# Kernel tuning notes

Hardware: AMD Instinct MI355X
Metric: run time of the kernel (lower is better)

Reference implementation:

```python
import jax, jax.numpy as jnp
import numpy as np

B, T, C = 4, 2048, 2048
H, KV, HD = 16, 4, 128  # n_head, n_kv_head, head_dim
G = H // KV             # query heads per kv head


def _rope(t, cos, sin):
    # t: [B, T, h, HD]; cos/sin: [T, HD//2] -> broadcast as [1, T, 1, HD//2]
    tr = t.reshape(t.shape[:-1] + (HD // 2, 2))
    t_r, t_i = tr[..., 0], tr[..., 1]
    c = cos[None, :, None, :]
    s = sin[None, :, None, :]
    o_r = t_r * c - t_i * s
    o_i = t_r * s + t_i * c
    return jnp.stack((o_r, o_i), axis=-1).reshape(t.shape)


def setup_inputs() -> dict:
    key = jax.random.key(0)
    ks = jax.random.split(key, 7)
    sc = 0.02
    return {
        "x": jax.random.normal(ks[0], (B, T, C), jnp.float32),
        "cos_freqs": jnp.cos(jnp.outer(jnp.arange(T, dtype=jnp.float32),
                                       1.0 / (10000.0 ** (jnp.arange(HD // 2, dtype=jnp.float32) * 2 / HD)))),
        "sin_freqs": jnp.sin(jnp.outer(jnp.arange(T, dtype=jnp.float32),
                                       1.0 / (10000.0 ** (jnp.arange(HD // 2, dtype=jnp.float32) * 2 / HD)))),
        "wq": jax.random.normal(ks[1], (H * HD, C), jnp.float32) * sc,
        "wk": jax.random.normal(ks[2], (KV * HD, C), jnp.float32) * sc,
        "wv": jax.random.normal(ks[3], (KV * HD, C), jnp.float32) * sc,
        "wo": jax.random.normal(ks[4], (C, H * HD), jnp.float32) * sc,
    }


def reference(x, cos_freqs, sin_freqs, wq, wk, wv, wo):
    # projections (Linear with bias=False: y = x @ W.T)
    q = (x @ wq.T).reshape(B, T, H, HD)
    k = (x @ wk.T).reshape(B, T, KV, HD)
    v = (x @ wv.T).reshape(B, T, KV, HD)
    q, k = _rope(q, cos_freqs, sin_freqs), _rope(k, cos_freqs, sin_freqs)
    # GQA attention without materializing repeated K/V: group q heads per kv head
    qg = q.reshape(B, T, KV, G, HD).transpose(0, 2, 3, 1, 4)  # [B,KV,G,T,HD]
    kh = k.transpose(0, 2, 1, 3)                              # [B,KV,T,HD]
    vh = v.transpose(0, 2, 1, 3)                              # [B,KV,T,HD]
    scale = 1.0 / jnp.sqrt(jnp.float32(HD))
    scores = jnp.einsum('bkgtd,bksd->bkgts', qg, kh) * scale  # [B,KV,G,T,T]
    mask = jnp.tril(jnp.ones((T, T), dtype=bool))
    scores = jnp.where(mask, scores, jnp.float32(-jnp.inf))
    attn = jax.nn.softmax(scores, axis=-1)
    out = jnp.einsum('bkgts,bksd->bkgtd', attn, vh)           # [B,KV,G,T,HD]
    out = out.transpose(0, 3, 1, 2, 4).reshape(B, T, H * HD)
    return out @ wo.T
```

## Files before the change

kernel.cpp:

```cpp
#include <hip/hip_runtime.h>
#include <hip/hip_bf16.h>
#include <math.h>

typedef __attribute__((ext_vector_type(8))) short short8;
typedef __attribute__((ext_vector_type(4))) float floatx4;

__device__ __forceinline__ float bf2f(unsigned short u) {
  union { unsigned int i; float f; } x; x.i = ((unsigned int)u) << 16; return x.f;
}
__device__ __forceinline__ unsigned short f2bf(float f) {
  union { float f; unsigned int i; } x; x.f = f;
  unsigned int r = x.i + 0x7FFFu + ((x.i >> 16) & 1u);
  return (unsigned short)(r >> 16);
}
__device__ __forceinline__ unsigned int pack2bf(float a, float b) {
  return (unsigned int)f2bf(a) | ((unsigned int)f2bf(b) << 16);
}
__device__ __forceinline__ void gl16(const void* g, void* l) {
  __builtin_amdgcn_global_load_lds(
      (const __attribute__((address_space(1))) unsigned int*)g,
      (__attribute__((address_space(3))) unsigned int*)l, 16, 0, 0);
}

__global__ void cvt_f32_bf16(const float* __restrict__ in, unsigned short* __restrict__ out, int n4) {
  int i = blockIdx.x * blockDim.x + threadIdx.x;
  if (i >= n4) return;
  float4 v = ((const float4*)in)[i];
  ushort4 o;
  o.x = f2bf(v.x); o.y = f2bf(v.y); o.z = f2bf(v.z); o.w = f2bf(v.w);
  ((ushort4*)out)[i] = o;
}

template<int MODE>
__global__ __launch_bounds__(256, 3) void gemm_bt(const unsigned short* __restrict__ A,
                                                  const unsigned short* __restrict__ Bw,
                                                  void* __restrict__ out0,
                                                  unsigned short* __restrict__ vtg,
                                                  int M, int N, int K, int nbx) {
  __shared__ __align__(16) unsigned short SM[24576];
  const int nb = gridDim.x;
  const int bid = blockIdx.x;
  const int tile = (bid & 7) * (nb >> 3) + (bid >> 3);
  const int n0 = (tile % nbx) * 128, m0 = (tile / nbx) * 128;
  const int tid = threadIdx.x;
  const int lane = tid & 63, wave = tid >> 6;
  const int wm = wave >> 1, wn = wave & 1;
  const int r = lane & 15, g = lane >> 4;
  const int swzr = (r >> 1) & 3;

  const int scg = (tid & 3) ^ ((tid >> 3) & 3);
  const unsigned short* Arow = A + (size_t)(m0 + (tid >> 2)) * K + scg * 8;
  const unsigned short* Brow = Bw + (size_t)(n0 + (tid >> 2)) * K + scg * 8;
  const size_t K64 = (size_t)K * 64;
  char* Lw = (char*)SM + wave * 1024;

  const int aoff = (wm * 64 + r) * 32 + ((g ^ swzr) << 3);
  const int boff = 4096 + (wn * 64 + r) * 32 + ((g ^ swzr) << 3);

  auto STAGE = [&](int slot, int t) {
    const unsigned short* Ag = Arow + ((size_t)t << 5);
    const unsigned short* Bg = Brow + ((size_t)t << 5);
    char* L = Lw + slot * 16384;
    gl16(Ag,       L);
    gl16(Ag + K64, L + 4096);
    gl16(Bg,       L + 8192);
    gl16(Bg + K64, L + 12288);
  };

  floatx4 acc[4][4] = {};
  const int NT = K >> 5;

  STAGE(0, 0);
  STAGE(1, 1);
  asm volatile("s_waitcnt vmcnt(4)" ::: "memory");
  __builtin_amdgcn_s_barrier();
  asm volatile("" ::: "memory");

  int rd = 0, st = 2;
  for (int t = 0; t < NT; ++t) {
    const unsigned short* Ls = SM + rd * 8192;
    short8 af[4], bf[4];
#pragma unroll
    for (int i = 0; i < 4; ++i) af[i] = *(const short8*)&Ls[aoff + i * 512];
#pragma unroll
    for (int j = 0; j < 4; ++j) bf[j] = *(const short8*)&Ls[boff + j * 512];
    if (t + 2 < NT) {
      STAGE(st, t + 2);
      asm volatile("s_waitcnt vmcnt(4)" ::: "memory");
    } else if (t + 1 < NT) {
      asm volatile("s_waitcnt vmcnt(0)" ::: "memory");
    }
    __builtin_amdgcn_s_barrier();
    asm volatile("" ::: "memory");
    __builtin_amdgcn_s_setprio(1);
#pragma unroll
    for (int i = 0; i < 4; ++i)
#pragma unroll
      for (int j = 0; j < 4; ++j)
        acc[i][j] = __builtin_amdgcn_mfma_f32_16x16x32_bf16(af[i], bf[j], acc[i][j], 0, 0, 0);
    __builtin_amdgcn_s_setprio(0);
    asm volatile("" ::: "memory");
    __builtin_amdgcn_s_barrier();
    asm volatile("" ::: "memory");
    rd = rd == 2 ? 0 : rd + 1;
    st = st == 2 ? 0 : st + 1;
  }

  if (MODE == 0) {
    float* SMf = (float*)SM;
    float* outp = (float*)out0;
#pragma unroll
    for (int p = 0; p < 4; ++p) {
      __syncthreads();
      if (wm == (p >> 1)) {
#pragma unroll
        for (int i2 = 0; i2 < 2; ++i2) {
          int i = (p & 1) * 2 + i2;
#pragma unroll
          for (int j = 0; j < 4; ++j)
#pragma unroll
            for (int q = 0; q < 4; ++q)
              SMf[(i2 * 16 + g * 4 + q) * 128 + wn * 64 + j * 16 + r] = acc[i][j][q];
        }
      }
      __syncthreads();
#pragma unroll
      for (int it = 0; it < 4; ++it) {
        int c = it * 256 + tid;
        int row = c >> 5, c4 = c & 31;
        float4 v = *(float4*)&SMf[row * 128 + c4 * 4];
        *(float4*)(outp + (size_t)(m0 + p * 32 + row) * N + n0 + c4 * 4) = v;
      }
    }
  } else if (n0 < 2560) {
    unsigned short* outp = (unsigned short*)out0;
#pragma unroll
    for (int p = 0; p < 4; ++p) {
      __syncthreads();
      if (wm == (p >> 1)) {
#pragma unroll
        for (int i2 = 0; i2 < 2; ++i2) {
          int i = (p & 1) * 2 + i2;
#pragma unroll
          for (int j = 0; j < 4; ++j)
#pragma unroll
            for (int q = 0; q < 4; ++q)
              SM[(i2 * 16 + g * 4 + q) * 128 + wn * 64 + j * 16 + r] = f2bf(acc[i][j][q]);
        }
      }
      __syncthreads();
#pragma unroll
      for (int it = 0; it < 2; ++it) {
        int c = it * 256 + tid;
        int row = c >> 4, c8 = c & 15;
        short8 v = *(short8*)&SM[row * 128 + c8 * 8];
        *(short8*)(outp + (size_t)(m0 + p * 32 + row) * N + n0 + c8 * 8) = v;
      }
    }
  } else {
#pragma unroll
    for (int p = 0; p < 2; ++p) {
      __syncthreads();
      if (wn == p) {
#pragma unroll
        for (int i = 0; i < 4; ++i)
#pragma unroll
          for (int j = 0; j < 4; ++j)
#pragma unroll
            for (int q = 0; q < 4; ++q) {
              int ml = wm * 64 + i * 16 + g * 4 + q;
              int nl = j * 16 + r;
              SM[nl * 128 + (((ml >> 3) ^ (nl & 7)) << 3) + (ml & 7)] = f2bf(acc[i][j][q]);
            }
      }
      __syncthreads();
#pragma unroll
      for (int it = 0; it < 4; ++it) {
        int c = it * 256 + tid;
        int nl = c >> 4, m8 = c & 15;
        short8 v = *(short8*)&SM[nl * 128 + ((m8 ^ (nl & 7)) << 3)];
        *(short8*)(vtg + (size_t)(n0 - 2560 + p * 64 + nl) * 8192 + m0 + m8 * 8) = v;
      }
    }
  }
}

__global__ void rope_inplace(unsigned short* __restrict__ t,
                             const float* __restrict__ cosf, const float* __restrict__ sinf,
                             int heads, int rowStride, int total, float scale) {
  int i = blockIdx.x * blockDim.x + threadIdx.x;
  if (i >= total) return;
  int d8 = i & 15;
  int rem = i >> 4;
  int head = rem % heads;
  int tok = rem / heads;
  int tpos = tok & 2047;
  unsigned short* p = t + (size_t)tok * rowStride + head * 128 + d8 * 8;
  short8 v = *(short8*)p;
  float4 c = *(const float4*)(cosf + (size_t)tpos * 64 + d8 * 4);
  float4 s = *(const float4*)(sinf + (size_t)tpos * 64 + d8 * 4);
  float cc[4] = {c.x, c.y, c.z, c.w};
  float ss[4] = {s.x, s.y, s.z, s.w};
  short8 o;
#pragma unroll
  for (int j = 0; j < 4; ++j) {
    float tr = bf2f((unsigned short)v[2 * j]);
    float ti = bf2f((unsigned short)v[2 * j + 1]);
    float orr = (tr * cc[j] - ti * ss[j]) * scale;
    float oi  = (tr * ss[j] + ti * cc[j]) * scale;
    o[2 * j]     = (short)f2bf(orr);
    o[2 * j + 1] = (short)f2bf(oi);
  }
  *(short8*)p = o;
}

__global__ __launch_bounds__(256, 2) void attn_fwd(const unsigned short* __restrict__ QKV,
                                                   const unsigned short* __restrict__ VT,
                                                   unsigned short* __restrict__ O) {
  constexpr int T = 2048;
  constexpr int LDQ = 3072;
  constexpr float NEG = -1e30f;
  __shared__ unsigned short Ks[2][64 * 128];
  __shared__ unsigned short Vs[2][128 * 64];
  const int gid = blockIdx.x;
  const int hb  = gid & 63;
  const int p   = gid >> 6;
  const int h = hb & 15, b = hb >> 4;
  const int kvh = h >> 2;
  const int tid = threadIdx.x, lane = tid & 63, w = tid >> 6;
  const int r = lane & 15, g = lane >> 4;
  const int rbase = (r & 3) + ((r >> 2) << 3);
  const int swzr  = (r & 3) | (((r >> 2) & 1) << 2);
  const size_t bT = (size_t)b * T;

  const unsigned short* Kgb = QKV + bT * LDQ + 2048 + kvh * 128;
  const unsigned short* Vgb = VT + (size_t)(kvh * 128) * 8192 + b * 2048;

  auto STAGE = [&](int bi, int kv0) {
#pragma unroll
    for (int t2 = 0; t2 < 4; ++t2) {
      int ck = w * 4 + t2;
      { int row = ck * 4 + (lane >> 4); int c16 = lane & 15;
        int swz = (row & 3) | (((row >> 3) & 1) << 2);
        gl16(Kgb + (size_t)(kv0 + row) * LDQ + ((c16 ^ swz) << 3),
             (char*)(&Ks[bi][0]) + ck * 1024); }
      { int row = ck * 8 + (lane >> 3); int c16 = lane & 7;
        gl16(Vgb + (size_t)row * 8192 + kv0 + ((c16 ^ (row & 7)) << 3),
             (char*)(&Vs[bi][0]) + ck * 1024); }
    }
  };

  for (int seg = 0; seg < 2; ++seg) {
    const int qb = seg ? p : 15 - p;
    const int q0 = qb * 128;

    short8 qf[2][4];
#pragma unroll
    for (int qt = 0; qt < 2; ++qt) {
      const unsigned short* qp = QKV + (bT + q0 + w * 32 + qt * 16 + r) * LDQ + h * 128;
#pragma unroll
      for (int c = 0; c < 4; ++c) qf[qt][c] = *(const short8*)(qp + c * 32 + g * 8);
    }

    floatx4 acc[8][2] = {};
    float mrun[2] = {NEG, NEG};
    float lrun[2] = {0.f, 0.f};

    const int ntiles = (q0 + 128) >> 6;
    STAGE(0, 0);
    asm volatile("s_waitcnt vmcnt(0)" ::: "memory");
    __syncthreads();

    for (int t = 0; t < ntiles; ++t) {
      const int cur = t & 1;
      const int kv0 = t << 6;
      if (t + 1 < ntiles) STAGE(cur ^ 1, (t + 1) << 6);

      if (kv0 <= q0 + w * 32 + 31) {
        floatx4 st[2][4] = {};
        __builtin_amdgcn_s_setprio(1);
#pragma unroll
        for (int c = 0; c < 4; ++c) {
          short8 kf[4];
#pragma unroll
          for (int kt = 0; kt < 4; ++kt) {
            const int row = rbase + ((kt & 1) << 2) + ((kt >> 1) << 5);
            kf[kt] = *(const short8*)&Ks[cur][row * 128 + (((g + 4 * c) ^ swzr) << 3)];
          }
#pragma unroll
          for (int qt = 0; qt < 2; ++qt)
#pragma unroll
            for (int kt = 0; kt < 4; ++kt)
              st[qt][kt] = __builtin_amdgcn_mfma_f32_16x16x32_bf16(kf[kt], qf[qt][c], st[qt][kt], 0, 0, 0);
        }
        __builtin_amdgcn_s_setprio(0);

        short8 va[2][8];
#pragma unroll
        for (int kc = 0; kc < 2; ++kc)
#pragma unroll
          for (int dt = 0; dt < 8; ++dt)
            va[kc][dt] = *(const short8*)&Vs[cur][(dt * 16 + r) * 64 + (((g + 4 * kc) ^ (r & 7)) << 3)];

#pragma unroll
        for (int qt = 0; qt < 2; ++qt) {
          const int qmin = q0 + w * 32 + qt * 16;
          const int qrow = qmin + r;
          float x[4][4];
          bool needmask = (kv0 + 64 > qmin);
#pragma unroll
          for (int kt = 0; kt < 4; ++kt) {
            const int kvb = kv0 + ((kt >> 1) << 5) + (g << 3) + ((kt & 1) << 2);
#pragma unroll
            for (int j = 0; j < 4; ++j) {
              float v = st[qt][kt][j];
              if (needmask) v = (kvb + j <= qrow) ? v : NEG;
              x[kt][j] = v;
            }
          }
          float mloc = x[0][0];
#pragma unroll
          for (int kt = 0; kt < 4; ++kt)
#pragma unroll
            for (int j = 0; j < 4; ++j) mloc = fmaxf(mloc, x[kt][j]);
          mloc = fmaxf(mloc, __shfl_xor(mloc, 16));
          mloc = fmaxf(mloc, __shfl_xor(mloc, 32));
          if (!__all(mloc <= mrun[qt] + 8.f)) {
            float mnew = fmaxf(mrun[qt], mloc);
            float al = __expf(mrun[qt] - mnew);
            mrun[qt] = mnew;
            lrun[qt] *= al;
#pragma unroll
            for (int dt = 0; dt < 8; ++dt) acc[dt][qt] *= al;
          }
          float pr[4][4], ssum = 0.f;
#pragma unroll
          for (int kt = 0; kt < 4; ++kt)
#pragma unroll
            for (int j = 0; j < 4; ++j) { pr[kt][j] = __expf(x[kt][j] - mrun[qt]); ssum += pr[kt][j]; }
          ssum += __shfl_xor(ssum, 16);
          ssum += __shfl_xor(ssum, 32);
          lrun[qt] += ssum;
          uint2 pk[4];
#pragma unroll
          for (int kt = 0; kt < 4; ++kt) {
            pk[kt].x = pack2bf(pr[kt][0], pr[kt][1]);
            pk[kt].y = pack2bf(pr[kt][2], pr[kt][3]);
          }
          __builtin_amdgcn_s_setprio(1);
#pragma unroll
          for (int kc = 0; kc < 2; ++kc) {
            union { unsigned int u[4]; short8 s; } bw;
            bw.u[0] = pk[2 * kc].x;
            bw.u[1] = pk[2 * kc].y;
            bw.u[2] = pk[2 * kc + 1].x;
            bw.u[3] = pk[2 * kc + 1].y;
#pragma unroll
            for (int dt = 0; dt < 8; ++dt)
              acc[dt][qt] = __builtin_amdgcn_mfma_f32_16x16x32_bf16(va[kc][dt], bw.s, acc[dt][qt], 0, 0, 0);
          }
          __builtin_amdgcn_s_setprio(0);
        }
      }

      asm volatile("s_waitcnt vmcnt(0)" ::: "memory");
      __syncthreads();
    }

#pragma unroll
    for (int qt = 0; qt < 2; ++qt) {
      float inv = 1.f / lrun[qt];
      unsigned short* op = O + (bT + q0 + w * 32 + qt * 16 + r) * 2048 + h * 128;
#pragma unroll
      for (int dt = 0; dt < 8; ++dt) {
        uint2 pkd;
        pkd.x = pack2bf(acc[dt][qt][0] * inv, acc[dt][qt][1] * inv);
        pkd.y = pack2bf(acc[dt][qt][2] * inv, acc[dt][qt][3] * inv);
        *(uint2*)(op + dt * 16 + g * 4) = pkd;
      }
    }
  }
}

extern "C" void kernel_launch(void* const* d_in, const int* in_sizes, int n_in,
                              void* d_out, int out_size, void* d_ws, size_t ws_size,
                              hipStream_t stream) {
  const float* x    = (const float*)d_in[0];
  const float* cosf = (const float*)d_in[1];
  const float* sinf = (const float*)d_in[2];
  const float* wq   = (const float*)d_in[3];
  const float* wk   = (const float*)d_in[4];
  const float* wv   = (const float*)d_in[5];
  const float* wo   = (const float*)d_in[6];

  unsigned short* xb   = (unsigned short*)d_ws;
  unsigned short* qkvw = xb   + 16777216;
  unsigned short* wob  = qkvw + 6291456;
  unsigned short* qkv  = wob  + 4194304;
  unsigned short* Vtg  = qkv  + 25165824;
  unsigned short* AO   = Vtg  + 4194304;

  cvt_f32_bf16<<<16384, 256, 0, stream>>>(x,  xb,  4194304);
  cvt_f32_bf16<<<4096,  256, 0, stream>>>(wq, qkvw,           1048576);
  cvt_f32_bf16<<<1024,  256, 0, stream>>>(wk, qkvw + 4194304, 262144);
  cvt_f32_bf16<<<1024,  256, 0, stream>>>(wv, qkvw + 5242880, 262144);
  cvt_f32_bf16<<<4096,  256, 0, stream>>>(wo, wob, 1048576);

  gemm_bt<1><<<1536, 256, 0, stream>>>(xb, qkvw, qkv, Vtg, 8192, 3072, 2048, 24);

  rope_inplace<<<8192, 256, 0, stream>>>(qkv,        cosf, sinf, 16, 3072, 2097152, 0.08838834764831845f);
  rope_inplace<<<2048, 256, 0, stream>>>(qkv + 2048, cosf, sinf, 4,  3072, 524288,  1.0f);

  attn_fwd<<<512, 256, 0, stream>>>(qkv, Vtg, AO);

  gemm_bt<0><<<1024, 256, 0, stream>>>(AO, wob, d_out, nullptr, 8192, 2048, 2048, 16);
}
```

Before: 387.8 us.

## Enlarge GEMM tiles to 256x256 with 8 waves and interleaved LDS reads

Moves the projection GEMMs from 128x128 tiles with 4 waves to 256x256 tiles with 8 waves, using double-buffered LDS in place of triple buffering. The MFMA sweep is split into four phases, each with its own barrier, so A-fragment LDS reads interleave with compute. The aim is more data reuse per loaded byte and less global traffic per FLOP. In exchange, grids get smaller (384 and 256 blocks), which may leave CUs underfilled or cause tail effects, and the extra barriers plus 128 accumulator registers per thread limit occupancy.

Result: faster. 371.1 us (-4.3%).

```diff
diff --git a/kernel.cpp b/kernel.cpp
--- a/kernel.cpp
+++ b/kernel.cpp
@@ -32,42 +32,42 @@
 }
 
 template<int MODE>
-__global__ __launch_bounds__(256, 3) void gemm_bt(const unsigned short* __restrict__ A,
+__global__ __launch_bounds__(512, 2) void gemm_bt(const unsigned short* __restrict__ A,
                                                   const unsigned short* __restrict__ Bw,
                                                   void* __restrict__ out0,
                                                   unsigned short* __restrict__ vtg,
                                                   int M, int N, int K, int nbx) {
-  __shared__ __align__(16) unsigned short SM[24576];
+  __shared__ __align__(16) unsigned short SM[32768];
   const int nb = gridDim.x;
   const int bid = blockIdx.x;
   const int tile = (bid & 7) * (nb >> 3) + (bid >> 3);
-  const int n0 = (tile % nbx) * 128, m0 = (tile / nbx) * 128;
+  const int n0 = (tile % nbx) * 256, m0 = (tile / nbx) * 256;
   const int tid = threadIdx.x;
   const int lane = tid & 63, wave = tid >> 6;
-  const int wm = wave >> 1, wn = wave & 1;
+  const int wm = wave >> 2, wn = wave & 3;
   const int r = lane & 15, g = lane >> 4;
   const int swzr = (r >> 1) & 3;
 
   const int scg = (tid & 3) ^ ((tid >> 3) & 3);
-  const unsigned short* Arow = A + (size_t)(m0 + (tid >> 2)) * K + scg * 8;
-  const unsigned short* Brow = Bw + (size_t)(n0 + (tid >> 2)) * K + scg * 8;
-  const size_t K64 = (size_t)K * 64;
-  char* Lw = (char*)SM + wave * 1024;
-
-  const int aoff = (wm * 64 + r) * 32 + ((g ^ swzr) << 3);
-  const int boff = 4096 + (wn * 64 + r) * 32 + ((g ^ swzr) << 3);
-
-  auto STAGE = [&](int slot, int t) {
-    const unsigned short* Ag = Arow + ((size_t)t << 5);
-    const unsigned short* Bg = Brow + ((size_t)t << 5);
-    char* L = Lw + slot * 16384;
-    gl16(Ag,       L);
-    gl16(Ag + K64, L + 4096);
-    gl16(Bg,       L + 8192);
-    gl16(Bg + K64, L + 12288);
+  const unsigned short* Ag0 = A  + (size_t)(m0 + (tid >> 2)) * K + scg * 8;
+  const unsigned short* Bg0 = Bw + (size_t)(n0 + (tid >> 2)) * K + scg * 8;
+  const size_t K128 = (size_t)K * 128;
+  char* const SMb = (char*)SM;
+
+  const int aoff = wm * 4096 + r * 32 + ((g ^ swzr) << 3);
+  const int boff = 16384 + (wn >> 1) * 4096 + ((wn & 1) * 64 + r) * 32 + ((g ^ swzr) << 3);
+
+  auto STAGE = [&](int s, int t) {
+    const size_t ko = (size_t)t << 5;
+    char* dA = SMb + s * 16384 + wave * 1024;
+    char* dB = SMb + 32768 + s * 16384 + wave * 1024;
+    gl16(Ag0 + ko,        dA);
+    gl16(Ag0 + K128 + ko, dA + 8192);
+    gl16(Bg0 + ko,        dB);
+    gl16(Bg0 + K128 + ko, dB + 8192);
   };
 
-  floatx4 acc[4][4] = {};
+  floatx4 acc[8][4] = {};
   const int NT = K >> 5;
 
   STAGE(0, 0);
@@ -76,16 +76,57 @@
   __builtin_amdgcn_s_barrier();
   asm volatile("" ::: "memory");
 
-  int rd = 0, st = 2;
   for (int t = 0; t < NT; ++t) {
-    const unsigned short* Ls = SM + rd * 8192;
-    short8 af[4], bf[4];
-#pragma unroll
-    for (int i = 0; i < 4; ++i) af[i] = *(const short8*)&Ls[aoff + i * 512];
-#pragma unroll
-    for (int j = 0; j < 4; ++j) bf[j] = *(const short8*)&Ls[boff + j * 512];
+    const int s = t & 1;
+    const unsigned short* Ls = SM + s * 8192;
+
+    short8 bfr[4];
+#pragma unroll
+    for (int j = 0; j < 4; ++j) bfr[j] = *(const short8*)&Ls[boff + j * 512];
+    short8 af0 = *(const short8*)&Ls[aoff];
+    short8 af1 = *(const short8*)&Ls[aoff + 512];
+    __builtin_amdgcn_s_barrier();
+    asm volatile("" ::: "memory");
+    __builtin_amdgcn_s_setprio(1);
+#pragma unroll
+    for (int j = 0; j < 4; ++j) {
+      acc[0][j] = __builtin_amdgcn_mfma_f32_16x16x32_bf16(af0, bfr[j], acc[0][j], 0, 0, 0);
+      acc[1][j] = __builtin_amdgcn_mfma_f32_16x16x32_bf16(af1, bfr[j], acc[1][j], 0, 0, 0);
+    }
+    __builtin_amdgcn_s_setprio(0);
+
+    short8 af2 = *(const short8*)&Ls[aoff + 2 * 512];
+    short8 af3 = *(const short8*)&Ls[aoff + 3 * 512];
+    __builtin_amdgcn_s_barrier();
+    asm volatile("" ::: "memory");
+    __builtin_amdgcn_s_setprio(1);
+#pragma unroll
+    for (int j = 0; j < 4; ++j) {
+      acc[2][j] = __builtin_amdgcn_mfma_f32_16x16x32_bf16(af2, bfr[j], acc[2][j], 0, 0, 0);
+      acc[3][j] = __builtin_amdgcn_mfma_f32_16x16x32_bf16(af3, bfr[j], acc[3][j], 0, 0, 0);
+    }
+    __builtin_amdgcn_s_setprio(0);
+
+    short8 af4 = *(const short8*)&Ls[aoff + 4 * 512];
+    short8 af5 = *(const short8*)&Ls[aoff + 5 * 512];
+    __builtin_amdgcn_s_barrier();
+    asm volatile("" ::: "memory");
+    __builtin_amdgcn_s_setprio(1);
+#pragma unroll
+    for (int j = 0; j < 4; ++j) {
+      acc[4][j] = __builtin_amdgcn_mfma_f32_16x16x32_bf16(af4, bfr[j], acc[4][j], 0, 0, 0);
+      acc[5][j] = __builtin_amdgcn_mfma_f32_16x16x32_bf16(af5, bfr[j], acc[5][j], 0, 0, 0);
+    }
+    __builtin_amdgcn_s_setprio(0);
+
+    short8 af6 = *(const short8*)&Ls[aoff + 6 * 512];
+    short8 af7 = *(const short8*)&Ls[aoff + 7 * 512];
+    asm volatile("s_waitcnt lgkmcnt(0)" ::: "memory");
+    __builtin_amdgcn_sched_barrier(0);
+    __builtin_amdgcn_s_barrier();
+    asm volatile("" ::: "memory");
     if (t + 2 < NT) {
-      STAGE(st, t + 2);
+      STAGE(s, t + 2);
       asm volatile("s_waitcnt vmcnt(4)" ::: "memory");
     } else if (t + 1 < NT) {
       asm volatile("s_waitcnt vmcnt(0)" ::: "memory");
@@ -94,92 +135,83 @@
     asm volatile("" ::: "memory");
     __builtin_amdgcn_s_setprio(1);
 #pragma unroll
-    for (int i = 0; i < 4; ++i)
-#pragma unroll
-      for (int j = 0; j < 4; ++j)
-        acc[i][j] = __builtin_amdgcn_mfma_f32_16x16x32_bf16(af[i], bf[j], acc[i][j], 0, 0, 0);
+    for (int j = 0; j < 4; ++j) {
+      acc[6][j] = __builtin_amdgcn_mfma_f32_16x16x32_bf16(af6, bfr[j], acc[6][j], 0, 0, 0);
+      acc[7][j] = __builtin_amdgcn_mfma_f32_16x16x32_bf16(af7, bfr[j], acc[7][j], 0, 0, 0);
+    }
     __builtin_amdgcn_s_setprio(0);
-    asm volatile("" ::: "memory");
-    __builtin_amdgcn_s_barrier();
-    asm volatile("" ::: "memory");
-    rd = rd == 2 ? 0 : rd + 1;
-    st = st == 2 ? 0 : st + 1;
   }
 
   if (MODE == 0) {
     float* SMf = (float*)SM;
     float* outp = (float*)out0;
 #pragma unroll
-    for (int p = 0; p < 4; ++p) {
-      __syncthreads();
-      if (wm == (p >> 1)) {
-#pragma unroll
-        for (int i2 = 0; i2 < 2; ++i2) {
-          int i = (p & 1) * 2 + i2;
+    for (int sp = 0; sp < 4; ++sp) {
+      __syncthreads();
+      if (wn == sp) {
+#pragma unroll
+        for (int i = 0; i < 8; ++i)
 #pragma unroll
           for (int j = 0; j < 4; ++j)
 #pragma unroll
             for (int q = 0; q < 4; ++q)
-              SMf[(i2 * 16 + g * 4 + q) * 128 + wn * 64 + j * 16 + r] = acc[i][j][q];
-        }
-      }
-      __syncthreads();
-#pragma unroll
-      for (int it = 0; it < 4; ++it) {
-        int c = it * 256 + tid;
-        int row = c >> 5, c4 = c & 31;
-        float4 v = *(float4*)&SMf[row * 128 + c4 * 4];
-        *(float4*)(outp + (size_t)(m0 + p * 32 + row) * N + n0 + c4 * 4) = v;
+              SMf[(wm * 128 + i * 16 + g * 4 + q) * 64 + j * 16 + r] = acc[i][j][q];
+      }
+      __syncthreads();
+#pragma unroll
+      for (int it = 0; it < 8; ++it) {
+        int c = it * 512 + tid;
+        int ml = c >> 4, c4 = c & 15;
+        float4 v = *(float4*)&SMf[ml * 64 + c4 * 4];
+        *(float4*)(outp + (size_t)(m0 + ml) * N + n0 + sp * 64 + c4 * 4) = v;
       }
     }
   } else if (n0 < 2560) {
     unsigned short* outp = (unsigned short*)out0;
 #pragma unroll
-    for (int p = 0; p < 4; ++p) {
-      __syncthreads();
-      if (wm == (p >> 1)) {
-#pragma unroll
-        for (int i2 = 0; i2 < 2; ++i2) {
-          int i = (p & 1) * 2 + i2;
+    for (int sp = 0; sp < 2; ++sp) {
+      __syncthreads();
+      if (wm == sp) {
+#pragma unroll
+        for (int i = 0; i < 8; ++i)
 #pragma unroll
           for (int j = 0; j < 4; ++j)
 #pragma unroll
             for (int q = 0; q < 4; ++q)
-              SM[(i2 * 16 + g * 4 + q) * 128 + wn * 64 + j * 16 + r] = f2bf(acc[i][j][q]);
-        }
-      }
-      __syncthreads();
-#pragma unroll
-      for (int it = 0; it < 2; ++it) {
-        int c = it * 256 + tid;
-        int row = c >> 4, c8 = c & 15;
-        short8 v = *(short8*)&SM[row * 128 + c8 * 8];
-        *(short8*)(outp + (size_t)(m0 + p * 32 + row) * N + n0 + c8 * 8) = v;
+              SM[(i * 16 + g * 4 + q) * 256 + wn * 64 + j * 16 + r] = f2bf(acc[i][j][q]);
+      }
+      __syncthreads();
+#pragma unroll
+      for (int it = 0; it < 8; ++it) {
+        int c = it * 512 + tid;
+        int ml = c >> 5, c8 = c & 31;
+        short8 v = *(short8*)&SM[ml * 256 + c8 * 8];
+        *(short8*)(outp + (size_t)(m0 + sp * 128 + ml) * N + n0 + c8 * 8) = v;
       }
     }
   } else {
 #pragma unroll
-    for (int p = 0; p < 2; ++p) {
-      __syncthreads();
-      if (wn == p) {
-#pragma unroll
-        for (int i = 0; i < 4; ++i)
+    for (int sp = 0; sp < 8; ++sp) {
+      __syncthreads();
+      if (wave == sp) {
+#pragma unroll
+        for (int i = 0; i < 8; ++i)
 #pragma unroll
           for (int j = 0; j < 4; ++j)
 #pragma unroll
             for (int q = 0; q < 4; ++q) {
-              int ml = wm * 64 + i * 16 + g * 4 + q;
+              int ml = i * 16 + g * 4 + q;
               int nl = j * 16 + r;
               SM[nl * 128 + (((ml >> 3) ^ (nl & 7)) << 3) + (ml & 7)] = f2bf(acc[i][j][q]);
             }
       }
       __syncthreads();
 #pragma unroll
-      for (int it = 0; it < 4; ++it) {
-        int c = it * 256 + tid;
+      for (int it = 0; it < 2; ++it) {
+        int c = it * 512 + tid;
         int nl = c >> 4, m8 = c & 15;
         short8 v = *(short8*)&SM[nl * 128 + ((m8 ^ (nl & 7)) << 3)];
-        *(short8*)(vtg + (size_t)(n0 - 2560 + p * 64 + nl) * 8192 + m0 + m8 * 8) = v;
+        *(short8*)(vtg + (size_t)(n0 - 2560 + (sp & 3) * 64 + nl) * 8192 + m0 + (sp >> 2) * 128 + m8 * 8) = v;
       }
     }
   }
@@ -406,12 +438,12 @@
   cvt_f32_bf16<<<1024,  256, 0, stream>>>(wv, qkvw + 5242880, 262144);
   cvt_f32_bf16<<<4096,  256, 0, stream>>>(wo, wob, 1048576);
 
-  gemm_bt<1><<<1536, 256, 0, stream>>>(xb, qkvw, qkv, Vtg, 8192, 3072, 2048, 24);
+  gemm_bt<1><<<384, 512, 0, stream>>>(xb, qkvw, qkv, Vtg, 8192, 3072, 2048, 12);
 
   rope_inplace<<<8192, 256, 0, stream>>>(qkv,        cosf, sinf, 16, 3072, 2097152, 0.08838834764831845f);
   rope_inplace<<<2048, 256, 0, stream>>>(qkv + 2048, cosf, sinf, 4,  3072, 524288,  1.0f);
 
   attn_fwd<<<512, 256, 0, stream>>>(qkv, Vtg, AO);
 
-  gemm_bt<0><<<1024, 256, 0, stream>>>(AO, wob, d_out, nullptr, 8192, 2048, 2048, 16);
-}
+  gemm_bt<0><<<256, 512, 0, stream>>>(AO, wob, d_out, nullptr, 8192, 2048, 2048, 8);
+}
```

## Restructure GEMM to double-buffered split-MFMA pipeline and unpair attention query blocks

Applied to the files above, without the earlier changes.

The GEMM main loop drops from a triple-buffered LDS ring with two barriers per step to a double buffer with one barrier. MFMA work is split into two halves so that the next tile's LDS fragment loads overlap the second half of the math, and LDS use falls from 48KB to 32KB. The attention kernel no longer pairs a long and a short query block in one workgroup to balance causal work. It launches one workgroup per query block (1024 instead of 512), ordered longest first, relying on the hardware scheduler for balance instead. The GEMM now waits for vmcnt(0) on each step, which exposes more global-load latency, and the attention split adds Q-load and setup overhead per block.

Result: slower. 396.3 us (+2.2%).

```diff
diff --git a/kernel.cpp b/kernel.cpp
--- a/kernel.cpp
+++ b/kernel.cpp
@@ -37,7 +37,7 @@
                                                   void* __restrict__ out0,
                                                   unsigned short* __restrict__ vtg,
                                                   int M, int N, int K, int nbx) {
-  __shared__ __align__(16) unsigned short SM[24576];
+  __shared__ __align__(16) unsigned short SM[16384];
   const int nb = gridDim.x;
   const int bid = blockIdx.x;
   const int tile = (bid & 7) * (nb >> 3) + (bid >> 3);
@@ -49,10 +49,10 @@
   const int swzr = (r >> 1) & 3;
 
   const int scg = (tid & 3) ^ ((tid >> 3) & 3);
-  const unsigned short* Arow = A + (size_t)(m0 + (tid >> 2)) * K + scg * 8;
+  const unsigned short* Arow = A  + (size_t)(m0 + (tid >> 2)) * K + scg * 8;
   const unsigned short* Brow = Bw + (size_t)(n0 + (tid >> 2)) * K + scg * 8;
   const size_t K64 = (size_t)K * 64;
-  char* Lw = (char*)SM + wave * 1024;
+  char* const Lw = (char*)SM + wave * 1024;
 
   const int aoff = (wm * 64 + r) * 32 + ((g ^ swzr) << 3);
   const int boff = 4096 + (wn * 64 + r) * 32 + ((g ^ swzr) << 3);
@@ -71,39 +71,56 @@
   const int NT = K >> 5;
 
   STAGE(0, 0);
-  STAGE(1, 1);
-  asm volatile("s_waitcnt vmcnt(4)" ::: "memory");
+  asm volatile("s_waitcnt vmcnt(0)" ::: "memory");
   __builtin_amdgcn_s_barrier();
   asm volatile("" ::: "memory");
 
-  int rd = 0, st = 2;
+  short8 bf[4], af01[2];
+#pragma unroll
+  for (int j = 0; j < 4; ++j) bf[j] = *(const short8*)&SM[boff + j * 512];
+#pragma unroll
+  for (int k = 0; k < 2; ++k) af01[k] = *(const short8*)&SM[aoff + k * 512];
+
   for (int t = 0; t < NT; ++t) {
-    const unsigned short* Ls = SM + rd * 8192;
-    short8 af[4], bf[4];
-#pragma unroll
-    for (int i = 0; i < 4; ++i) af[i] = *(const short8*)&Ls[aoff + i * 512];
-#pragma unroll
-    for (int j = 0; j < 4; ++j) bf[j] = *(const short8*)&Ls[boff + j * 512];
-    if (t + 2 < NT) {
-      STAGE(st, t + 2);
-      asm volatile("s_waitcnt vmcnt(4)" ::: "memory");
-    } else if (t + 1 < NT) {
-      asm volatile("s_waitcnt vmcnt(0)" ::: "memory");
-    }
+    const int s = t & 1;
+    const unsigned short* Ls = SM + s * 8192;
+    const unsigned short* Ln = SM + (s ^ 1) * 8192;
+    const bool pf = (t + 1 < NT);
+    short8 af23[2], bfN[4], afN[2];
+
+#pragma unroll
+    for (int k = 0; k < 2; ++k) af23[k] = *(const short8*)&Ls[aoff + (2 + k) * 512];
+    if (pf) STAGE(s ^ 1, t + 1);
+    __builtin_amdgcn_s_setprio(1);
+#pragma unroll
+    for (int j = 0; j < 4; ++j) {
+      acc[0][j] = __builtin_amdgcn_mfma_f32_16x16x32_bf16(af01[0], bf[j], acc[0][j], 0, 0, 0);
+      acc[1][j] = __builtin_amdgcn_mfma_f32_16x16x32_bf16(af01[1], bf[j], acc[1][j], 0, 0, 0);
+    }
+    __builtin_amdgcn_s_setprio(0);
+
+    asm volatile("s_waitcnt lgkmcnt(0)" ::: "memory");
+    if (pf) asm volatile("s_waitcnt vmcnt(0)" ::: "memory");
     __builtin_amdgcn_s_barrier();
     asm volatile("" ::: "memory");
+    if (pf) {
+#pragma unroll
+      for (int j = 0; j < 4; ++j) bfN[j] = *(const short8*)&Ln[boff + j * 512];
+#pragma unroll
+      for (int k = 0; k < 2; ++k) afN[k] = *(const short8*)&Ln[aoff + k * 512];
+    }
     __builtin_amdgcn_s_setprio(1);
 #pragma unroll
-    for (int i = 0; i < 4; ++i)
-#pragma unroll
-      for (int j = 0; j < 4; ++j)
-        acc[i][j] = __builtin_amdgcn_mfma_f32_16x16x32_bf16(af[i], bf[j], acc[i][j], 0, 0, 0);
+    for (int j = 0; j < 4; ++j) {
+      acc[2][j] = __builtin_amdgcn_mfma_f32_16x16x32_bf16(af23[0], bf[j], acc[2][j], 0, 0, 0);
+      acc[3][j] = __builtin_amdgcn_mfma_f32_16x16x32_bf16(af23[1], bf[j], acc[3][j], 0, 0, 0);
+    }
     __builtin_amdgcn_s_setprio(0);
-    asm volatile("" ::: "memory");
-    __builtin_amdgcn_s_barrier();
-    asm volatile("" ::: "memory");
-    rd = rd == 2 ? 0 : rd + 1;
-    st = st == 2 ? 0 : st + 1;
+    if (pf) {
+#pragma unroll
+      for (int j = 0; j < 4; ++j) bf[j] = bfN[j];
+      af01[0] = afN[0]; af01[1] = afN[1];
+    }
   }
 
   if (MODE == 0) {
@@ -224,7 +241,7 @@
   __shared__ unsigned short Vs[2][128 * 64];
   const int gid = blockIdx.x;
   const int hb  = gid & 63;
-  const int p   = gid >> 6;
+  const int qb  = 15 - (gid >> 6);
   const int h = hb & 15, b = hb >> 4;
   const int kvh = h >> 2;
   const int tid = threadIdx.x, lane = tid & 63, w = tid >> 6;
@@ -250,134 +267,131 @@
     }
   };
 
-  for (int seg = 0; seg < 2; ++seg) {
-    const int qb = seg ? p : 15 - p;
-    const int q0 = qb * 128;
-
-    short8 qf[2][4];
-#pragma unroll
-    for (int qt = 0; qt < 2; ++qt) {
-      const unsigned short* qp = QKV + (bT + q0 + w * 32 + qt * 16 + r) * LDQ + h * 128;
-#pragma unroll
-      for (int c = 0; c < 4; ++c) qf[qt][c] = *(const short8*)(qp + c * 32 + g * 8);
-    }
-
-    floatx4 acc[8][2] = {};
-    float mrun[2] = {NEG, NEG};
-    float lrun[2] = {0.f, 0.f};
-
-    const int ntiles = (q0 + 128) >> 6;
-    STAGE(0, 0);
+  const int q0 = qb * 128;
+
+  short8 qf[2][4];
+#pragma unroll
+  for (int qt = 0; qt < 2; ++qt) {
+    const unsigned short* qp = QKV + (bT + q0 + w * 32 + qt * 16 + r) * LDQ + h * 128;
+#pragma unroll
+    for (int c = 0; c < 4; ++c) qf[qt][c] = *(const short8*)(qp + c * 32 + g * 8);
+  }
+
+  floatx4 acc[8][2] = {};
+  float mrun[2] = {NEG, NEG};
+  float lrun[2] = {0.f, 0.f};
+
+  const int ntiles = (q0 + 128) >> 6;
+  STAGE(0, 0);
+  asm volatile("s_waitcnt vmcnt(0)" ::: "memory");
+  __syncthreads();
+
+  for (int t = 0; t < ntiles; ++t) {
+    const int cur = t & 1;
+    const int kv0 = t << 6;
+    if (t + 1 < ntiles) STAGE(cur ^ 1, (t + 1) << 6);
+
+    if (kv0 <= q0 + w * 32 + 31) {
+      floatx4 st[2][4] = {};
+      __builtin_amdgcn_s_setprio(1);
+#pragma unroll
+      for (int c = 0; c < 4; ++c) {
+        short8 kf[4];
+#pragma unroll
+        for (int kt = 0; kt < 4; ++kt) {
+          const int row = rbase + ((kt & 1) << 2) + ((kt >> 1) << 5);
+          kf[kt] = *(const short8*)&Ks[cur][row * 128 + (((g + 4 * c) ^ swzr) << 3)];
+        }
+#pragma unroll
+        for (int qt = 0; qt < 2; ++qt)
+#pragma unroll
+          for (int kt = 0; kt < 4; ++kt)
+            st[qt][kt] = __builtin_amdgcn_mfma_f32_16x16x32_bf16(kf[kt], qf[qt][c], st[qt][kt], 0, 0, 0);
+      }
+      __builtin_amdgcn_s_setprio(0);
+
+      short8 va[2][8];
+#pragma unroll
+      for (int kc = 0; kc < 2; ++kc)
+#pragma unroll
+        for (int dt = 0; dt < 8; ++dt)
+          va[kc][dt] = *(const short8*)&Vs[cur][(dt * 16 + r) * 64 + (((g + 4 * kc) ^ (r & 7)) << 3)];
+
+#pragma unroll
+      for (int qt = 0; qt < 2; ++qt) {
+        const int qmin = q0 + w * 32 + qt * 16;
+        const int qrow = qmin + r;
+        float x[4][4];
+        bool needmask = (kv0 + 64 > qmin);
+#pragma unroll
+        for (int kt = 0; kt < 4; ++kt) {
+          const int kvb = kv0 + ((kt >> 1) << 5) + (g << 3) + ((kt & 1) << 2);
+#pragma unroll
+          for (int j = 0; j < 4; ++j) {
+            float v = st[qt][kt][j];
+            if (needmask) v = (kvb + j <= qrow) ? v : NEG;
+            x[kt][j] = v;
+          }
+        }
+        float mloc = x[0][0];
+#pragma unroll
+        for (int kt = 0; kt < 4; ++kt)
+#pragma unroll
+          for (int j = 0; j < 4; ++j) mloc = fmaxf(mloc, x[kt][j]);
+        mloc = fmaxf(mloc, __shfl_xor(mloc, 16));
+        mloc = fmaxf(mloc, __shfl_xor(mloc, 32));
+        if (!__all(mloc <= mrun[qt] + 8.f)) {
+          float mnew = fmaxf(mrun[qt], mloc);
+          float al = __expf(mrun[qt] - mnew);
+          mrun[qt] = mnew;
+          lrun[qt] *= al;
+#pragma unroll
+          for (int dt = 0; dt < 8; ++dt) acc[dt][qt] *= al;
+        }
+        float pr[4][4], ssum = 0.f;
+#pragma unroll
+        for (int kt = 0; kt < 4; ++kt)
+#pragma unroll
+          for (int j = 0; j < 4; ++j) { pr[kt][j] = __expf(x[kt][j] - mrun[qt]); ssum += pr[kt][j]; }
+        ssum += __shfl_xor(ssum, 16);
+        ssum += __shfl_xor(ssum, 32);
+        lrun[qt] += ssum;
+        uint2 pk[4];
+#pragma unroll
+        for (int kt = 0; kt < 4; ++kt) {
+          pk[kt].x = pack2bf(pr[kt][0], pr[kt][1]);
+          pk[kt].y = pack2bf(pr[kt][2], pr[kt][3]);
+        }
+        __builtin_amdgcn_s_setprio(1);
+#pragma unroll
+        for (int kc = 0; kc < 2; ++kc) {
+          union { unsigned int u[4]; short8 s; } bw;
+          bw.u[0] = pk[2 * kc].x;
+          bw.u[1] = pk[2 * kc].y;
+          bw.u[2] = pk[2 * kc + 1].x;
+          bw.u[3] = pk[2 * kc + 1].y;
+#pragma unroll
+          for (int dt = 0; dt < 8; ++dt)
+            acc[dt][qt] = __builtin_amdgcn_mfma_f32_16x16x32_bf16(va[kc][dt], bw.s, acc[dt][qt], 0, 0, 0);
+        }
+        __builtin_amdgcn_s_setprio(0);
+      }
+    }
+
     asm volatile("s_waitcnt vmcnt(0)" ::: "memory");
     __syncthreads();
-
-    for (int t = 0; t < ntiles; ++t) {
-      const int cur = t & 1;
-      const int kv0 = t << 6;
-      if (t + 1 < ntiles) STAGE(cur ^ 1, (t + 1) << 6);
-
-      if (kv0 <= q0 + w * 32 + 31) {
-        floatx4 st[2][4] = {};
-        __builtin_amdgcn_s_setprio(1);
-#pragma unroll
-        for (int c = 0; c < 4; ++c) {
-          short8 kf[4];
-#pragma unroll
-          for (int kt = 0; kt < 4; ++kt) {
-            const int row = rbase + ((kt & 1) << 2) + ((kt >> 1) << 5);
-            kf[kt] = *(const short8*)&Ks[cur][row * 128 + (((g + 4 * c) ^ swzr) << 3)];
-          }
-#pragma unroll
-          for (int qt = 0; qt < 2; ++qt)
-#pragma unroll
-            for (int kt = 0; kt < 4; ++kt)
-              st[qt][kt] = __builtin_amdgcn_mfma_f32_16x16x32_bf16(kf[kt], qf[qt][c], st[qt][kt], 0, 0, 0);
-        }
-        __builtin_amdgcn_s_setprio(0);
-
-        short8 va[2][8];
-#pragma unroll
-        for (int kc = 0; kc < 2; ++kc)
-#pragma unroll
-          for (int dt = 0; dt < 8; ++dt)
-            va[kc][dt] = *(const short8*)&Vs[cur][(dt * 16 + r) * 64 + (((g + 4 * kc) ^ (r & 7)) << 3)];
-
-#pragma unroll
-        for (int qt = 0; qt < 2; ++qt) {
-          const int qmin = q0 + w * 32 + qt * 16;
-          const int qrow = qmin + r;
-          float x[4][4];
-          bool needmask = (kv0 + 64 > qmin);
-#pragma unroll
-          for (int kt = 0; kt < 4; ++kt) {
-            const int kvb = kv0 + ((kt >> 1) << 5) + (g << 3) + ((kt & 1) << 2);
-#pragma unroll
-            for (int j = 0; j < 4; ++j) {
-              float v = st[qt][kt][j];
-              if (needmask) v = (kvb + j <= qrow) ? v : NEG;
-              x[kt][j] = v;
-            }
-          }
-          float mloc = x[0][0];
-#pragma unroll
-          for (int kt = 0; kt < 4; ++kt)
-#pragma unroll
-            for (int j = 0; j < 4; ++j) mloc = fmaxf(mloc, x[kt][j]);
-          mloc = fmaxf(mloc, __shfl_xor(mloc, 16));
-          mloc = fmaxf(mloc, __shfl_xor(mloc, 32));
-          if (!__all(mloc <= mrun[qt] + 8.f)) {
-            float mnew = fmaxf(mrun[qt], mloc);
-            float al = __expf(mrun[qt] - mnew);
-            mrun[qt] = mnew;
-            lrun[qt] *= al;
-#pragma unroll
-            for (int dt = 0; dt < 8; ++dt) acc[dt][qt] *= al;
-          }
-          float pr[4][4], ssum = 0.f;
-#pragma unroll
-          for (int kt = 0; kt < 4; ++kt)
-#pragma unroll
-            for (int j = 0; j < 4; ++j) { pr[kt][j] = __expf(x[kt][j] - mrun[qt]); ssum += pr[kt][j]; }
-          ssum += __shfl_xor(ssum, 16);
-          ssum += __shfl_xor(ssum, 32);
-          lrun[qt] += ssum;
-          uint2 pk[4];
-#pragma unroll
-          for (int kt = 0; kt < 4; ++kt) {
-            pk[kt].x = pack2bf(pr[kt][0], pr[kt][1]);
-            pk[kt].y = pack2bf(pr[kt][2], pr[kt][3]);
-          }
-          __builtin_amdgcn_s_setprio(1);
-#pragma unroll
-          for (int kc = 0; kc < 2; ++kc) {
-            union { unsigned int u[4]; short8 s; } bw;
-            bw.u[0] = pk[2 * kc].x;
-            bw.u[1] = pk[2 * kc].y;
-            bw.u[2] = pk[2 * kc + 1].x;
-            bw.u[3] = pk[2 * kc + 1].y;
-#pragma unroll
-            for (int dt = 0; dt < 8; ++dt)
-              acc[dt][qt] = __builtin_amdgcn_mfma_f32_16x16x32_bf16(va[kc][dt], bw.s, acc[dt][qt], 0, 0, 0);
-          }
-          __builtin_amdgcn_s_setprio(0);
-        }
-      }
-
-      asm volatile("s_waitcnt vmcnt(0)" ::: "memory");
-      __syncthreads();
-    }
-
-#pragma unroll
-    for (int qt = 0; qt < 2; ++qt) {
-      float inv = 1.f / lrun[qt];
-      unsigned short* op = O + (bT + q0 + w * 32 + qt * 16 + r) * 2048 + h * 128;
-#pragma unroll
-      for (int dt = 0; dt < 8; ++dt) {
-        uint2 pkd;
-        pkd.x = pack2bf(acc[dt][qt][0] * inv, acc[dt][qt][1] * inv);
-        pkd.y = pack2bf(acc[dt][qt][2] * inv, acc[dt][qt][3] * inv);
-        *(uint2*)(op + dt * 16 + g * 4) = pkd;
-      }
+  }
+
+#pragma unroll
+  for (int qt = 0; qt < 2; ++qt) {
+    float inv = 1.f / lrun[qt];
+    unsigned short* op = O + (bT + q0 + w * 32 + qt * 16 + r) * 2048 + h * 128;
+#pragma unroll
+    for (int dt = 0; dt < 8; ++dt) {
+      uint2 pkd;
+      pkd.x = pack2bf(acc[dt][qt][0] * inv, acc[dt][qt][1] * inv);
+      pkd.y = pack2bf(acc[dt][qt][2] * inv, acc[dt][qt][3] * inv);
+      *(uint2*)(op + dt * 16 + g * 4) = pkd;
     }
   }
 }
@@ -411,7 +425,7 @@
   rope_inplace<<<8192, 256, 0, stream>>>(qkv,        cosf, sinf, 16, 3072, 2097152, 0.08838834764831845f);
   rope_inplace<<<2048, 256, 0, stream>>>(qkv + 2048, cosf, sinf, 4,  3072, 524288,  1.0f);
 
-  attn_fwd<<<512, 256, 0, stream>>>(qkv, Vtg, AO);
+  attn_fwd<<<1024, 256, 0, stream>>>(qkv, Vtg, AO);
 
   gemm_bt<0><<<1024, 256, 0, stream>>>(AO, wob, d_out, nullptr, 8192, 2048, 2048, 16);
 }
```
